# Kernel optimization log

Measured on AMD Instinct MI355X. Metric: run time of the kernel, lower is better.

Reference implementation:

```python
import jax, jax.numpy as jnp
import numpy as np

PROX_THRESH = 50.0
NEG_SLOPE = 0.2  # PyG GATConv default leaky_relu slope


def _layer_norm(x, g, b, eps=1e-5):
    m = x.mean(-1, keepdims=True)
    v = x.var(-1, keepdims=True)
    return (x - m) / jnp.sqrt(v + eps) * g + b


def _forward(ego_agent_past, neighbor_agents_past, node_w, node_b, node_ln_g,
             node_ln_b, ego_w, ego_b, ego_ln_g, ego_ln_b, gat_w, gat_asrc,
             gat_adst, gat_b, proj_w, proj_b):
    B = ego_agent_past.shape[0]
    ego_last = ego_agent_past[:, -1, :5]            # [B,5]
    nbr_last = neighbor_agents_past[:, :, -1, :5]   # [B,Nn,5]
    x = jnp.concatenate([ego_last[:, None], nbr_last], axis=1)  # [B,N,5]
    N = x.shape[1]
    dim = node_w.shape[1]
    heads, C = gat_asrc.shape[1], gat_asrc.shape[2]

    # build_graph: edge (j->i) iff dist(i,j) < 50 and i != j; GATConv then
    # adds self-loops, so the diagonal is always connected.
    pos = x[..., :2]
    d2 = jnp.sum((pos[:, :, None, :] - pos[:, None, :, :]) ** 2, axis=-1)  # [B,N,N]
    eye = jnp.eye(N, dtype=bool)
    adj = ((jnp.sqrt(d2) < PROX_THRESH) & ~eye) | eye   # adj[b,i,j]: msg j -> i

    # node features zero-padded from 5 -> 11 columns (as in forward)
    nf = jnp.pad(x, ((0, 0), (0, 0), (0, 11 - x.shape[-1])))
    h_node = _layer_norm(jax.nn.relu(nf @ node_w + node_b), node_ln_g, node_ln_b)
    h_ego = _layer_norm(jax.nn.relu(nf[..., :7] @ ego_w + ego_b), ego_ln_g, ego_ln_b)
    is_ego = (jnp.arange(N) == 0)  # node 0 of every scene is the ego
    h = jnp.where(is_ego[None, :, None], h_ego, h_node)  # [B,N,dim]

    # GATConv layers (eval mode, dropout inactive), concat=True
    for l in range(gat_w.shape[0]):
        wh = (h @ gat_w[l]).reshape(B, N, heads, C)                    # [B,N,H,C]
        a_s = jnp.einsum('bnhc,hc->bnh', wh, gat_asrc[l])              # source term
        a_d = jnp.einsum('bnhc,hc->bnh', wh, gat_adst[l])              # dest term
        # e[b,i,j,h] for edge j->i
        e = jax.nn.leaky_relu(a_s[:, None, :, :] + a_d[:, :, None, :], NEG_SLOPE)
        e = jnp.where(adj[..., None], e, -1e9)
        alpha = jax.nn.softmax(e, axis=2)                              # over sources j
        out = jnp.einsum('bijh,bjhc->bihc', alpha, wh).reshape(B, N, dim) + gat_b[l]
        h = jax.nn.relu(out)

    h = h @ proj_w + proj_b
    # all agents are valid (randn features have nonzero abs-sum), so no padding
    mask = jnp.zeros((B, N), dtype=bool)
    return h, mask


def setup_inputs() -> dict:
    key = jax.random.key(0)
    ks = jax.random.split(key, 10)
    B, Nn, T = 16, 1023, 20
    dim, heads, L = 256, 4, 2
    C = dim // heads
    f = lambda i, s: jax.random.normal(ks[i], s, dtype=jnp.float32)
    return {
        'ego_agent_past': f(0, (B, T, 7)),
        'neighbor_agents_past': f(1, (B, Nn, T, 11)),
        'node_w': f(2, (11, dim)) * 0.1, 'node_b': jnp.zeros((dim,), jnp.float32),
        'node_ln_g': jnp.ones((dim,), jnp.float32), 'node_ln_b': jnp.zeros((dim,), jnp.float32),
        'ego_w': f(3, (7, dim)) * 0.1, 'ego_b': jnp.zeros((dim,), jnp.float32),
        'ego_ln_g': jnp.ones((dim,), jnp.float32), 'ego_ln_b': jnp.zeros((dim,), jnp.float32),
        'gat_w': f(4, (L, dim, dim)) * 0.1,
        'gat_asrc': f(5, (L, heads, C)) * 0.1,
        'gat_adst': f(6, (L, heads, C)) * 0.1,
        'gat_b': jnp.zeros((L, dim), jnp.float32),
        'proj_w': f(7, (dim, dim)) * 0.1, 'proj_b': jnp.zeros((dim,), jnp.float32),
    }


def reference(ego_agent_past, neighbor_agents_past, node_w, node_b, node_ln_g,
              node_ln_b, ego_w, ego_b, ego_ln_g, ego_ln_b, gat_w, gat_asrc,
              gat_adst, gat_b, proj_w, proj_b):
    return _forward(ego_agent_past, neighbor_agents_past, node_w, node_b,
                    node_ln_g, node_ln_b, ego_w, ego_b, ego_ln_g, ego_ln_b,
                    gat_w, gat_asrc, gat_adst, gat_b, proj_w, proj_b)
```

## Files before the change

### kernel.cpp

```cpp
#include <hip/hip_runtime.h>
#include <cstddef>

typedef _Float16 f16;
typedef _Float16 f16x8 __attribute__((ext_vector_type(8)));
typedef _Float16 f16x4 __attribute__((ext_vector_type(4)));
typedef float f32x4 __attribute__((ext_vector_type(4)));

#define BATCH 16
#define NAGENT 1024
#define NNBR 1023
#define TSTEP 20
#define DIM 256
#define ROWS 16384
#define TH2 2500.0f
#define LOG2E 1.44269504089f

#define O_PX   0
#define O_PY   16384
#define O_H16  32768
#define O_AS   2129920
#define O_AD   2195456
#define O_M    2260992
#define O_US   2261056
#define O_UD   2263104
#define O_WT   2265152
#define O_ADJ  2363456

__global__ __launch_bounds__(256) void node_embed(
    const float* __restrict__ ego, const float* __restrict__ nbr,
    const float* __restrict__ node_w, const float* __restrict__ node_b,
    const float* __restrict__ node_g, const float* __restrict__ node_beta,
    const float* __restrict__ ego_w, const float* __restrict__ ego_b,
    const float* __restrict__ ego_g, const float* __restrict__ ego_beta,
    f16* __restrict__ h16, float* __restrict__ px, float* __restrict__ py) {
    int w = threadIdx.x >> 6, lane = threadIdx.x & 63;
    int row = blockIdx.x * 4 + w;
    int b = row >> 10, n = row & 1023;
    const float* src;
    if (n == 0) src = ego + (size_t)b * TSTEP * 7 + (TSTEP - 1) * 7;
    else        src = nbr + (((size_t)b * NNBR + (n - 1)) * TSTEP + (TSTEP - 1)) * 11;
    const float *W, *bias, *g, *beta;
    if (n == 0) { W = ego_w;  bias = ego_b;  g = ego_g;  beta = ego_beta; }
    else        { W = node_w; bias = node_b; g = node_g; beta = node_beta; }
    float xv[5];
#pragma unroll
    for (int k = 0; k < 5; k++) xv[k] = src[k];
    if (lane == 0) { px[row] = xv[0]; py[row] = xv[1]; }
    int c0 = lane * 4;
    float4 bv = *(const float4*)(bias + c0);
    float acc[4] = {bv.x, bv.y, bv.z, bv.w};
#pragma unroll
    for (int k = 0; k < 5; k++) {
        float4 wv = *(const float4*)(W + (size_t)k * 256 + c0);
        acc[0] = fmaf(xv[k], wv.x, acc[0]);
        acc[1] = fmaf(xv[k], wv.y, acc[1]);
        acc[2] = fmaf(xv[k], wv.z, acc[2]);
        acc[3] = fmaf(xv[k], wv.w, acc[3]);
    }
#pragma unroll
    for (int c = 0; c < 4; c++) acc[c] = fmaxf(acc[c], 0.f);
    float s1 = acc[0] + acc[1] + acc[2] + acc[3];
    float s2 = acc[0]*acc[0] + acc[1]*acc[1] + acc[2]*acc[2] + acc[3]*acc[3];
#pragma unroll
    for (int off = 1; off < 64; off <<= 1) {
        s1 += __shfl_xor(s1, off);
        s2 += __shfl_xor(s2, off);
    }
    float mean = s1 * (1.f / 256.f);
    float var  = s2 * (1.f / 256.f) - mean * mean;
    float rstd = rsqrtf(var + 1e-5f);
    float4 gv = *(const float4*)(g + c0);
    float4 be = *(const float4*)(beta + c0);
    f16x4 o;
    o[0] = (f16)((acc[0] - mean) * rstd * gv.x + be.x);
    o[1] = (f16)((acc[1] - mean) * rstd * gv.y + be.y);
    o[2] = (f16)((acc[2] - mean) * rstd * gv.z + be.z);
    o[3] = (f16)((acc[3] - mean) * rstd * gv.w + be.w);
    *(f16x4*)(h16 + (size_t)row * 256 + c0) = o;
}

__global__ __launch_bounds__(256) void adj_build(const float* __restrict__ px,
                                                 const float* __restrict__ py,
                                                 unsigned char* __restrict__ mask) {
    int blk = blockIdx.x;
    int b = blk >> 6, ic = blk & 63;
    int base = b << 10;
    __shared__ float sx[1024], sy[1024];
    int t = threadIdx.x;
#pragma unroll
    for (int i = 0; i < 4; i++) {
        sx[t + i * 256] = px[base + t + i * 256];
        sy[t + i * 256] = py[base + t + i * 256];
    }
    __syncthreads();
    int i_loc = t >> 4;
    int s = (t >> 3) & 1;
    int q = (t >> 1) & 3;
    int chalf = t & 1;
    int ig = ic * 16 + i_loc;
    float xi = sx[ig], yi = sy[ig];
    unsigned int w0 = 0, w1 = 0;
#pragma unroll
    for (int cc = 0; cc < 8; cc++) {
        int c = chalf * 8 + cc;
        unsigned int byte = 0;
        int j0 = s * 512 + c * 32 + q * 8;
#pragma unroll
        for (int jj = 0; jj < 8; jj++) {
            int j = j0 + jj;
            float dx = sx[j] - xi, dy = sy[j] - yi;
            if ((dx * dx + dy * dy < TH2) || (j == ig)) byte |= 1u << jj;
        }
        if (cc < 4) w0 |= byte << (cc * 8);
        else        w1 |= byte << ((cc - 4) * 8);
    }
    uint2 v; v.x = w0; v.y = w1;
    *(uint2*)(mask + (((size_t)(base + ig)) << 7) + s * 64 + q * 16 + chalf * 8) = v;
}

__global__ __launch_bounds__(256) void prep_weights(
    const float* __restrict__ gat_w, const float* __restrict__ proj_w,
    const float* __restrict__ asrc, const float* __restrict__ adst,
    f16* __restrict__ WT, float* __restrict__ us, float* __restrict__ ud) {
    int bid = blockIdx.x;
    int t = threadIdx.x;
    if (bid < 48) {
        int m = bid >> 4, t4 = bid & 15;
        int ti = (t4 >> 2) * 64;
        int tj = (t4 & 3) * 64;
        const float* W = (m < 2) ? (gat_w + (size_t)m * 65536) : proj_w;
        __shared__ float ls[64][68];
#pragma unroll
        for (int i = 0; i < 4; i++) {
            int idx = t + i * 256;
            int r = idx >> 4, c4 = (idx & 15) * 4;
            float4 v = *(const float4*)(W + (size_t)(ti + r) * 256 + tj + c4);
            ls[r][c4] = v.x; ls[r][c4 + 1] = v.y; ls[r][c4 + 2] = v.z; ls[r][c4 + 3] = v.w;
        }
        __syncthreads();
#pragma unroll
        for (int i = 0; i < 2; i++) {
            int idx = t + i * 256;
            int nr = idx >> 3, kc = (idx & 7) * 8;
            f16x8 v;
#pragma unroll
            for (int j = 0; j < 8; j++) v[j] = (f16)ls[kc + j][nr];
            *(f16x8*)(WT + (size_t)m * 65536 + (size_t)(tj + nr) * 256 + ti + kc) = v;
        }
    } else {
        int blk = bid - 48;
        int l = blk >> 2, h = blk & 3;
        const float* W  = gat_w + (size_t)l * 65536 + t * 256 + h * 64;
        const float* as = asrc + l * 256 + h * 64;
        const float* ad = adst + l * 256 + h * 64;
        float s = 0.f, d = 0.f;
#pragma unroll 8
        for (int c = 0; c < 64; c++) { s = fmaf(W[c], as[c], s); d = fmaf(W[c], ad[c], d); }
        us[blk * 256 + t] = s;
        ud[blk * 256 + t] = d;
    }
}

__global__ __launch_bounds__(256, 4) void gemm_f16(
    const f16* __restrict__ A, const f16* __restrict__ BT,
    f16* __restrict__ whT, float* __restrict__ outF, const float* __restrict__ bias,
    const float* __restrict__ us, const float* __restrict__ ud,
    float* __restrict__ a_sT, float* __restrict__ a_dT) {
    __shared__ f16 sA[32 * 264];
    __shared__ float sU[8 * 256];
    int t = threadIdx.x;
    int m0 = blockIdx.x * 32;
    {
        int r = t >> 3, u0 = (t & 7) * 4;
        const f16* gp = A + (size_t)(m0 + r) * 256 + u0 * 8;
        f16* lp = sA + r * 264 + u0 * 8;
#pragma unroll
        for (int u = 0; u < 4; u++)
            *(f16x8*)(lp + u * 8) = *(const f16x8*)(gp + u * 8);
    }
    if (us) {
#pragma unroll
        for (int i = 0; i < 4; i++) sU[t + i * 256] = us[t + i * 256];
#pragma unroll
        for (int i = 0; i < 4; i++) sU[1024 + t + i * 256] = ud[t + i * 256];
    }
    __syncthreads();
    int w = t >> 6, lane = t & 63, il = lane & 15, q = lane >> 4;
    int n0 = w * 64;
    f32x4 acc[2][4];
#pragma unroll
    for (int mt = 0; mt < 2; mt++)
#pragma unroll
        for (int nt = 0; nt < 4; nt++) acc[mt][nt] = (f32x4){0.f, 0.f, 0.f, 0.f};
    const f16* Bp  = BT + (size_t)(n0 + il) * 256 + q * 8;
    const f16* Ap0 = sA + il * 264 + q * 8;
#pragma unroll 2
    for (int ks = 0; ks < 256; ks += 32) {
        f16x8 a0 = *(const f16x8*)(Ap0 + ks);
        f16x8 a1 = *(const f16x8*)(Ap0 + 16 * 264 + ks);
        f16x8 b0 = *(const f16x8*)(Bp + ks);
        f16x8 b1 = *(const f16x8*)(Bp + 16 * 256 + ks);
        f16x8 b2 = *(const f16x8*)(Bp + 32 * 256 + ks);
        f16x8 b3 = *(const f16x8*)(Bp + 48 * 256 + ks);
        acc[0][0] = __builtin_amdgcn_mfma_f32_16x16x32_f16(a0, b0, acc[0][0], 0, 0, 0);
        acc[0][1] = __builtin_amdgcn_mfma_f32_16x16x32_f16(a0, b1, acc[0][1], 0, 0, 0);
        acc[0][2] = __builtin_amdgcn_mfma_f32_16x16x32_f16(a0, b2, acc[0][2], 0, 0, 0);
        acc[0][3] = __builtin_amdgcn_mfma_f32_16x16x32_f16(a0, b3, acc[0][3], 0, 0, 0);
        acc[1][0] = __builtin_amdgcn_mfma_f32_16x16x32_f16(a1, b0, acc[1][0], 0, 0, 0);
        acc[1][1] = __builtin_amdgcn_mfma_f32_16x16x32_f16(a1, b1, acc[1][1], 0, 0, 0);
        acc[1][2] = __builtin_amdgcn_mfma_f32_16x16x32_f16(a1, b2, acc[1][2], 0, 0, 0);
        acc[1][3] = __builtin_amdgcn_mfma_f32_16x16x32_f16(a1, b3, acc[1][3], 0, 0, 0);
    }
    if (whT) {
#pragma unroll
        for (int mt = 0; mt < 2; mt++)
#pragma unroll
            for (int nt = 0; nt < 4; nt++) {
                f16x4 v;
#pragma unroll
                for (int reg = 0; reg < 4; reg++) v[reg] = (f16)acc[mt][nt][reg];
                *(f16x4*)(whT + (size_t)(n0 + nt * 16 + il) * ROWS + m0 + mt * 16 + q * 4) = v;
            }
    } else {
#pragma unroll
        for (int nt = 0; nt < 4; nt++) {
            float bv = bias[n0 + nt * 16 + il];
#pragma unroll
            for (int mt = 0; mt < 2; mt++)
#pragma unroll
                for (int reg = 0; reg < 4; reg++)
                    outF[(size_t)(m0 + mt * 16 + q * 4 + reg) * 256 + n0 + nt * 16 + il] =
                        acc[mt][nt][reg] + bv;
        }
    }
    if (us) {
        int r2 = t >> 3, sub = t & 7;
        int hh = sub & 3, isD = sub >> 2;
        const float* uv = sU + isD * 1024 + hh * 256;
        const f16* ar = sA + r2 * 264;
        float d0 = 0.f;
#pragma unroll 4
        for (int kk = 0; kk < 32; kk++) {
            f16x8 av = *(const f16x8*)(ar + kk * 8);
            float4 u0 = *(const float4*)(uv + kk * 8);
            float4 u1 = *(const float4*)(uv + kk * 8 + 4);
            d0 += (float)av[0] * u0.x + (float)av[1] * u0.y +
                  (float)av[2] * u0.z + (float)av[3] * u0.w +
                  (float)av[4] * u1.x + (float)av[5] * u1.y +
                  (float)av[6] * u1.z + (float)av[7] * u1.w;
        }
        float* dst = isD ? a_dT : a_sT;
        dst[(size_t)hh * ROWS + m0 + r2] = d0;
    }
}

__global__ __launch_bounds__(256) void reduce_max(const float* __restrict__ a_sT,
                                                  float* __restrict__ M) {
    int blk = blockIdx.x;
    int b = blk >> 2, h = blk & 3;
    const float* p = a_sT + (size_t)h * ROWS + b * NAGENT;
    int t = threadIdx.x;
    float m = fmaxf(fmaxf(p[t], p[t + 256]), fmaxf(p[t + 512], p[t + 768]));
#pragma unroll
    for (int off = 32; off > 0; off >>= 1) m = fmaxf(m, __shfl_down(m, off));
    __shared__ float red[4];
    if ((t & 63) == 0) red[t >> 6] = m;
    __syncthreads();
    if (t == 0) M[blk] = fmaxf(fmaxf(red[0], red[1]), fmaxf(red[2], red[3]));
}

__global__ __launch_bounds__(512, 4) void gat_attn(
    const f16* __restrict__ whT, const float* __restrict__ a_sT,
    const float* __restrict__ a_dT, const unsigned char* __restrict__ mask,
    const float* __restrict__ M, const float* __restrict__ gat_b,
    f16* __restrict__ h16out) {
    __shared__ f32x4 comb[4][64][10];
    int t = threadIdx.x;
    int w = t >> 6, lane = t & 63;
    int h = w & 3, s = w >> 2;
    int blk = blockIdx.x;
    int b = blk >> 5;
    int i0 = (blk & 31) << 5;
    int base = b << 10;
    int il = lane & 15, q = lane >> 4;
    int ig0 = i0 + il, ig1 = i0 + 16 + il;

    float Mh = M[b * 4 + h];
    float adv0 = a_dT[(size_t)h * ROWS + base + ig0];
    float adv1 = a_dT[(size_t)h * ROWS + base + ig1];
    float mz0 = Mh + adv0, mz1 = Mh + adv1;
    float mi0 = fmaxf(mz0, 0.2f * mz0), mi1 = fmaxf(mz1, 0.2f * mz1);
    float nm0 = -mi0 * LOG2E, nm1 = -mi1 * LOG2E;

    uint4 mq0 = *(const uint4*)(mask + (((size_t)(base + ig0)) << 7) + s * 64 + q * 16);
    uint4 mq1 = *(const uint4*)(mask + (((size_t)(base + ig1)) << 7) + s * 64 + q * 16);
    unsigned int mw0[4] = {mq0.x, mq0.y, mq0.z, mq0.w};
    unsigned int mw1[4] = {mq1.x, mq1.y, mq1.z, mq1.w};

    f32x4 acc[2][5];
#pragma unroll
    for (int mt = 0; mt < 2; mt++)
#pragma unroll
        for (int nt = 0; nt < 5; nt++) acc[mt][nt] = (f32x4){0.f, 0.f, 0.f, 0.f};
    f16x8 ones;
#pragma unroll
    for (int j = 0; j < 8; j++) ones[j] = (f16)1.f;

    int jbase = base + (s << 9);
    const f16*   wp  = whT + (size_t)(h * 64 + il) * ROWS + jbase + q * 8;
    const float* asp = a_sT + (size_t)h * ROWS + jbase + q * 8;

    for (int c = 0; c < 16; ++c) {
        int j0 = c * 32;
        f16x8 b0 = *(const f16x8*)(wp + j0);
        f16x8 b1 = *(const f16x8*)(wp + (size_t)16 * ROWS + j0);
        f16x8 b2 = *(const f16x8*)(wp + (size_t)32 * ROWS + j0);
        f16x8 b3 = *(const f16x8*)(wp + (size_t)48 * ROWS + j0);
        float4 as0 = *(const float4*)(asp + j0);
        float4 as1 = *(const float4*)(asp + j0 + 4);
        unsigned int mb0 = (mw0[c >> 2] >> ((c & 3) * 8)) & 255u;
        unsigned int mb1 = (mw1[c >> 2] >> ((c & 3) * 8)) & 255u;
        float asv[8] = {as0.x, as0.y, as0.z, as0.w, as1.x, as1.y, as1.z, as1.w};
        f16x8 afr0, afr1;
#pragma unroll
        for (int jj = 0; jj < 8; ++jj) {
            float z = asv[jj];
            float z0 = z + adv0, z1 = z + adv1;
            float sc0 = fmaxf(z0, 0.2f * z0), sc1 = fmaxf(z1, 0.2f * z1);
            float e0 = exp2f(fmaf(sc0, LOG2E, nm0));
            float e1 = exp2f(fmaf(sc1, LOG2E, nm1));
            afr0[jj] = (f16)(((mb0 >> jj) & 1u) ? e0 : 0.f);
            afr1[jj] = (f16)(((mb1 >> jj) & 1u) ? e1 : 0.f);
        }
        acc[0][0] = __builtin_amdgcn_mfma_f32_16x16x32_f16(afr0, b0, acc[0][0], 0, 0, 0);
        acc[1][0] = __builtin_amdgcn_mfma_f32_16x16x32_f16(afr1, b0, acc[1][0], 0, 0, 0);
        acc[0][1] = __builtin_amdgcn_mfma_f32_16x16x32_f16(afr0, b1, acc[0][1], 0, 0, 0);
        acc[1][1] = __builtin_amdgcn_mfma_f32_16x16x32_f16(afr1, b1, acc[1][1], 0, 0, 0);
        acc[0][2] = __builtin_amdgcn_mfma_f32_16x16x32_f16(afr0, b2, acc[0][2], 0, 0, 0);
        acc[1][2] = __builtin_amdgcn_mfma_f32_16x16x32_f16(afr1, b2, acc[1][2], 0, 0, 0);
        acc[0][3] = __builtin_amdgcn_mfma_f32_16x16x32_f16(afr0, b3, acc[0][3], 0, 0, 0);
        acc[1][3] = __builtin_amdgcn_mfma_f32_16x16x32_f16(afr1, b3, acc[1][3], 0, 0, 0);
        acc[0][4] = __builtin_amdgcn_mfma_f32_16x16x32_f16(afr0, ones, acc[0][4], 0, 0, 0);
        acc[1][4] = __builtin_amdgcn_mfma_f32_16x16x32_f16(afr1, ones, acc[1][4], 0, 0, 0);
    }
    if (s == 1) {
#pragma unroll
        for (int mt = 0; mt < 2; mt++)
#pragma unroll
            for (int nt = 0; nt < 5; nt++) comb[h][lane][mt * 5 + nt] = acc[mt][nt];
    }
    __syncthreads();
    if (s == 0) {
#pragma unroll
        for (int mt = 0; mt < 2; mt++)
#pragma unroll
            for (int nt = 0; nt < 5; nt++) acc[mt][nt] += comb[h][lane][mt * 5 + nt];
        float b0v = gat_b[h * 64 + il];
        float b1v = gat_b[h * 64 + 16 + il];
        float b2v = gat_b[h * 64 + 32 + il];
        float b3v = gat_b[h * 64 + 48 + il];
#pragma unroll
        for (int mt = 0; mt < 2; mt++) {
#pragma unroll
            for (int reg = 0; reg < 4; ++reg) {
                float inv = 1.f / acc[mt][4][reg];
                size_t ro = (size_t)(base + i0 + mt * 16 + q * 4 + reg) * DIM + h * 64 + il;
                h16out[ro +  0] = (f16)fmaxf(fmaf(acc[mt][0][reg], inv, b0v), 0.f);
                h16out[ro + 16] = (f16)fmaxf(fmaf(acc[mt][1][reg], inv, b1v), 0.f);
                h16out[ro + 32] = (f16)fmaxf(fmaf(acc[mt][2][reg], inv, b2v), 0.f);
                h16out[ro + 48] = (f16)fmaxf(fmaf(acc[mt][3][reg], inv, b3v), 0.f);
            }
        }
    }
}

__global__ void zero_mask(float* __restrict__ p) {
    p[blockIdx.x * 256 + threadIdx.x] = 0.f;
}

extern "C" void kernel_launch(void* const* d_in, const int* in_sizes, int n_in,
                              void* d_out, int out_size, void* d_ws, size_t ws_size,
                              hipStream_t stream) {
    const float* ego       = (const float*)d_in[0];
    const float* nbr       = (const float*)d_in[1];
    const float* node_w    = (const float*)d_in[2];
    const float* node_b    = (const float*)d_in[3];
    const float* node_g    = (const float*)d_in[4];
    const float* node_beta = (const float*)d_in[5];
    const float* ego_w     = (const float*)d_in[6];
    const float* ego_b     = (const float*)d_in[7];
    const float* ego_g     = (const float*)d_in[8];
    const float* ego_beta  = (const float*)d_in[9];
    const float* gat_w     = (const float*)d_in[10];
    const float* gat_asrc  = (const float*)d_in[11];
    const float* gat_adst  = (const float*)d_in[12];
    const float* gat_bias  = (const float*)d_in[13];
    const float* proj_w    = (const float*)d_in[14];
    const float* proj_b    = (const float*)d_in[15];

    float* out = (float*)d_out;
    float* ws  = (float*)d_ws;
    float* px   = ws + O_PX;
    float* py   = ws + O_PY;
    f16*   h16  = (f16*)(ws + O_H16);
    float* asT  = ws + O_AS;
    float* adT  = ws + O_AD;
    float* Mmax = ws + O_M;
    float* us   = ws + O_US;
    float* ud   = ws + O_UD;
    f16*   WT   = (f16*)(ws + O_WT);
    unsigned char* adj = (unsigned char*)(ws + O_ADJ);
    f16*   whT  = (f16*)d_out;

    node_embed<<<4096, 256, 0, stream>>>(ego, nbr, node_w, node_b, node_g, node_beta,
                                         ego_w, ego_b, ego_g, ego_beta, h16, px, py);
    adj_build<<<1024, 256, 0, stream>>>(px, py, adj);
    prep_weights<<<56, 256, 0, stream>>>(gat_w, proj_w, gat_asrc, gat_adst, WT, us, ud);
    for (int l = 0; l < 2; l++) {
        gemm_f16<<<512, 256, 0, stream>>>(h16, WT + (size_t)l * 65536, whT, nullptr, nullptr,
                                          us + l * 1024, ud + l * 1024, asT, adT);
        reduce_max<<<64, 256, 0, stream>>>(asT, Mmax);
        gat_attn<<<512, 512, 0, stream>>>(whT, asT, adT, adj, Mmax,
                                          gat_bias + l * 256, h16);
    }
    gemm_f16<<<512, 256, 0, stream>>>(h16, WT + (size_t)2 * 65536, nullptr, out, proj_b,
                                      nullptr, nullptr, nullptr, nullptr);
    zero_mask<<<64, 256, 0, stream>>>(out + (size_t)ROWS * DIM);
}
```

Before: 252.4 us.

## Halve GEMM row tile, pack exp conversions, transpose attention combine buffer

The GEMM now gives each block 16 rows instead of 32 and launches 1024 blocks, which adds parallelism across CUs but loads each B tile twice as often. The attention softmax weights are converted in pairs with packed round-toward-zero f16 conversion instead of per-element casts. The shared combine buffer is transposed so that lanes access consecutive addresses, avoiding LDS bank conflicts. The rtz rounding slightly changes the numerics.

```diff
diff --git a/kernel.cpp b/kernel.cpp
--- a/kernel.cpp
+++ b/kernel.cpp
@@ -4,6 +4,7 @@
 typedef _Float16 f16;
 typedef _Float16 f16x8 __attribute__((ext_vector_type(8)));
 typedef _Float16 f16x4 __attribute__((ext_vector_type(4)));
+typedef __fp16 fp16x2 __attribute__((ext_vector_type(2)));
 typedef float f32x4 __attribute__((ext_vector_type(4)));
 
 #define BATCH 16
@@ -166,17 +167,16 @@
     f16* __restrict__ whT, float* __restrict__ outF, const float* __restrict__ bias,
     const float* __restrict__ us, const float* __restrict__ ud,
     float* __restrict__ a_sT, float* __restrict__ a_dT) {
-    __shared__ f16 sA[32 * 264];
+    __shared__ f16 sA[16 * 264];
     __shared__ float sU[8 * 256];
     int t = threadIdx.x;
-    int m0 = blockIdx.x * 32;
+    int m0 = blockIdx.x * 16;
     {
-        int r = t >> 3, u0 = (t & 7) * 4;
-        const f16* gp = A + (size_t)(m0 + r) * 256 + u0 * 8;
-        f16* lp = sA + r * 264 + u0 * 8;
-#pragma unroll
-        for (int u = 0; u < 4; u++)
-            *(f16x8*)(lp + u * 8) = *(const f16x8*)(gp + u * 8);
+        int r = t >> 4, u0 = (t & 15) * 16;
+        const f16* gp = A + (size_t)(m0 + r) * 256 + u0;
+        f16* lp = sA + r * 264 + u0;
+        *(f16x8*)lp = *(const f16x8*)gp;
+        *(f16x8*)(lp + 8) = *(const f16x8*)(gp + 8);
     }
     if (us) {
 #pragma unroll
@@ -187,70 +187,61 @@
     __syncthreads();
     int w = t >> 6, lane = t & 63, il = lane & 15, q = lane >> 4;
     int n0 = w * 64;
-    f32x4 acc[2][4];
-#pragma unroll
-    for (int mt = 0; mt < 2; mt++)
-#pragma unroll
-        for (int nt = 0; nt < 4; nt++) acc[mt][nt] = (f32x4){0.f, 0.f, 0.f, 0.f};
+    f32x4 acc[4];
+#pragma unroll
+    for (int nt = 0; nt < 4; nt++) acc[nt] = (f32x4){0.f, 0.f, 0.f, 0.f};
     const f16* Bp  = BT + (size_t)(n0 + il) * 256 + q * 8;
     const f16* Ap0 = sA + il * 264 + q * 8;
 #pragma unroll 2
     for (int ks = 0; ks < 256; ks += 32) {
         f16x8 a0 = *(const f16x8*)(Ap0 + ks);
-        f16x8 a1 = *(const f16x8*)(Ap0 + 16 * 264 + ks);
         f16x8 b0 = *(const f16x8*)(Bp + ks);
         f16x8 b1 = *(const f16x8*)(Bp + 16 * 256 + ks);
         f16x8 b2 = *(const f16x8*)(Bp + 32 * 256 + ks);
         f16x8 b3 = *(const f16x8*)(Bp + 48 * 256 + ks);
-        acc[0][0] = __builtin_amdgcn_mfma_f32_16x16x32_f16(a0, b0, acc[0][0], 0, 0, 0);
-        acc[0][1] = __builtin_amdgcn_mfma_f32_16x16x32_f16(a0, b1, acc[0][1], 0, 0, 0);
-        acc[0][2] = __builtin_amdgcn_mfma_f32_16x16x32_f16(a0, b2, acc[0][2], 0, 0, 0);
-        acc[0][3] = __builtin_amdgcn_mfma_f32_16x16x32_f16(a0, b3, acc[0][3], 0, 0, 0);
-        acc[1][0] = __builtin_amdgcn_mfma_f32_16x16x32_f16(a1, b0, acc[1][0], 0, 0, 0);
-        acc[1][1] = __builtin_amdgcn_mfma_f32_16x16x32_f16(a1, b1, acc[1][1], 0, 0, 0);
-        acc[1][2] = __builtin_amdgcn_mfma_f32_16x16x32_f16(a1, b2, acc[1][2], 0, 0, 0);
-        acc[1][3] = __builtin_amdgcn_mfma_f32_16x16x32_f16(a1, b3, acc[1][3], 0, 0, 0);
+        acc[0] = __builtin_amdgcn_mfma_f32_16x16x32_f16(a0, b0, acc[0], 0, 0, 0);
+        acc[1] = __builtin_amdgcn_mfma_f32_16x16x32_f16(a0, b1, acc[1], 0, 0, 0);
+        acc[2] = __builtin_amdgcn_mfma_f32_16x16x32_f16(a0, b2, acc[2], 0, 0, 0);
+        acc[3] = __builtin_amdgcn_mfma_f32_16x16x32_f16(a0, b3, acc[3], 0, 0, 0);
     }
     if (whT) {
 #pragma unroll
-        for (int mt = 0; mt < 2; mt++)
-#pragma unroll
-            for (int nt = 0; nt < 4; nt++) {
-                f16x4 v;
-#pragma unroll
-                for (int reg = 0; reg < 4; reg++) v[reg] = (f16)acc[mt][nt][reg];
-                *(f16x4*)(whT + (size_t)(n0 + nt * 16 + il) * ROWS + m0 + mt * 16 + q * 4) = v;
-            }
+        for (int nt = 0; nt < 4; nt++) {
+            f16x4 v;
+#pragma unroll
+            for (int reg = 0; reg < 4; reg++) v[reg] = (f16)acc[nt][reg];
+            *(f16x4*)(whT + (size_t)(n0 + nt * 16 + il) * ROWS + m0 + q * 4) = v;
+        }
     } else {
 #pragma unroll
         for (int nt = 0; nt < 4; nt++) {
             float bv = bias[n0 + nt * 16 + il];
 #pragma unroll
-            for (int mt = 0; mt < 2; mt++)
-#pragma unroll
-                for (int reg = 0; reg < 4; reg++)
-                    outF[(size_t)(m0 + mt * 16 + q * 4 + reg) * 256 + n0 + nt * 16 + il] =
-                        acc[mt][nt][reg] + bv;
+            for (int reg = 0; reg < 4; reg++)
+                outF[(size_t)(m0 + q * 4 + reg) * 256 + n0 + nt * 16 + il] =
+                    acc[nt][reg] + bv;
         }
     }
     if (us) {
-        int r2 = t >> 3, sub = t & 7;
-        int hh = sub & 3, isD = sub >> 2;
-        const float* uv = sU + isD * 1024 + hh * 256;
-        const f16* ar = sA + r2 * 264;
-        float d0 = 0.f;
+        int r2 = t >> 4, sub = t & 15;
+        if (sub < 8) {
+            int hh = sub & 3, isD = sub >> 2;
+            const float* uv = sU + isD * 1024 + hh * 256;
+            const f16* ar = sA + r2 * 264;
+            float d0 = 0.f;
 #pragma unroll 4
-        for (int kk = 0; kk < 32; kk++) {
-            f16x8 av = *(const f16x8*)(ar + kk * 8);
-            float4 u0 = *(const float4*)(uv + kk * 8);
-            float4 u1 = *(const float4*)(uv + kk * 8 + 4);
-            d0 += (float)av[0] * u0.x + (float)av[1] * u0.y +
-                  (float)av[2] * u0.z + (float)av[3] * u0.w +
-                  (float)av[4] * u1.x + (float)av[5] * u1.y +
-                  (float)av[6] * u1.z + (float)av[7] * u1.w;
-        }
-        float* dst = isD ? a_dT : a_sT;
-        dst[(size_t)hh * ROWS + m0 + r2] = d0;
+            for (int kk = 0; kk < 32; kk++) {
+                f16x8 av = *(const f16x8*)(ar + kk * 8);
+                float4 u0 = *(const float4*)(uv + kk * 8);
+                float4 u1 = *(const float4*)(uv + kk * 8 + 4);
+                d0 += (float)av[0] * u0.x + (float)av[1] * u0.y +
+                      (float)av[2] * u0.z + (float)av[3] * u0.w +
+                      (float)av[4] * u1.x + (float)av[5] * u1.y +
+                      (float)av[6] * u1.z + (float)av[7] * u1.w;
+            }
+            float* dst = isD ? a_dT : a_sT;
+            dst[(size_t)hh * ROWS + m0 + r2] = d0;
+        }
     }
 }
 
@@ -274,7 +265,7 @@
     const float* __restrict__ a_dT, const unsigned char* __restrict__ mask,
     const float* __restrict__ M, const float* __restrict__ gat_b,
     f16* __restrict__ h16out) {
-    __shared__ f32x4 comb[4][64][10];
+    __shared__ f32x4 comb[10][4][64];
     int t = threadIdx.x;
     int w = t >> 6, lane = t & 63;
     int h = w & 3, s = w >> 2;
@@ -321,17 +312,26 @@
         unsigned int mb0 = (mw0[c >> 2] >> ((c & 3) * 8)) & 255u;
         unsigned int mb1 = (mw1[c >> 2] >> ((c & 3) * 8)) & 255u;
         float asv[8] = {as0.x, as0.y, as0.z, as0.w, as1.x, as1.y, as1.z, as1.w};
-        f16x8 afr0, afr1;
-#pragma unroll
-        for (int jj = 0; jj < 8; ++jj) {
-            float z = asv[jj];
-            float z0 = z + adv0, z1 = z + adv1;
-            float sc0 = fmaxf(z0, 0.2f * z0), sc1 = fmaxf(z1, 0.2f * z1);
-            float e0 = exp2f(fmaf(sc0, LOG2E, nm0));
-            float e1 = exp2f(fmaf(sc1, LOG2E, nm1));
-            afr0[jj] = (f16)(((mb0 >> jj) & 1u) ? e0 : 0.f);
-            afr1[jj] = (f16)(((mb1 >> jj) & 1u) ? e1 : 0.f);
-        }
+        union { f16x8 v; fp16x2 hp[4]; } u0, u1;
+#pragma unroll
+        for (int jp = 0; jp < 4; ++jp) {
+            float va = asv[2 * jp], vb = asv[2 * jp + 1];
+            float za = va + adv0, zb = vb + adv0;
+            float zc = va + adv1, zd = vb + adv1;
+            float sa = fmaxf(za, 0.2f * za), sb = fmaxf(zb, 0.2f * zb);
+            float sc_ = fmaxf(zc, 0.2f * zc), sd = fmaxf(zd, 0.2f * zd);
+            float ea = exp2f(fmaf(sa, LOG2E, nm0));
+            float eb = exp2f(fmaf(sb, LOG2E, nm0));
+            float ec = exp2f(fmaf(sc_, LOG2E, nm1));
+            float ed = exp2f(fmaf(sd, LOG2E, nm1));
+            ea = ((mb0 >> (2 * jp)) & 1u) ? ea : 0.f;
+            eb = ((mb0 >> (2 * jp + 1)) & 1u) ? eb : 0.f;
+            ec = ((mb1 >> (2 * jp)) & 1u) ? ec : 0.f;
+            ed = ((mb1 >> (2 * jp + 1)) & 1u) ? ed : 0.f;
+            u0.hp[jp] = __builtin_amdgcn_cvt_pkrtz(ea, eb);
+            u1.hp[jp] = __builtin_amdgcn_cvt_pkrtz(ec, ed);
+        }
+        f16x8 afr0 = u0.v, afr1 = u1.v;
         acc[0][0] = __builtin_amdgcn_mfma_f32_16x16x32_f16(afr0, b0, acc[0][0], 0, 0, 0);
         acc[1][0] = __builtin_amdgcn_mfma_f32_16x16x32_f16(afr1, b0, acc[1][0], 0, 0, 0);
         acc[0][1] = __builtin_amdgcn_mfma_f32_16x16x32_f16(afr0, b1, acc[0][1], 0, 0, 0);
@@ -347,14 +347,14 @@
 #pragma unroll
         for (int mt = 0; mt < 2; mt++)
 #pragma unroll
-            for (int nt = 0; nt < 5; nt++) comb[h][lane][mt * 5 + nt] = acc[mt][nt];
+            for (int nt = 0; nt < 5; nt++) comb[mt * 5 + nt][h][lane] = acc[mt][nt];
     }
     __syncthreads();
     if (s == 0) {
 #pragma unroll
         for (int mt = 0; mt < 2; mt++)
 #pragma unroll
-            for (int nt = 0; nt < 5; nt++) acc[mt][nt] += comb[h][lane][mt * 5 + nt];
+            for (int nt = 0; nt < 5; nt++) acc[mt][nt] += comb[mt * 5 + nt][h][lane];
         float b0v = gat_b[h * 64 + il];
         float b1v = gat_b[h * 64 + 16 + il];
         float b2v = gat_b[h * 64 + 32 + il];
@@ -417,13 +417,13 @@
     adj_build<<<1024, 256, 0, stream>>>(px, py, adj);
     prep_weights<<<56, 256, 0, stream>>>(gat_w, proj_w, gat_asrc, gat_adst, WT, us, ud);
     for (int l = 0; l < 2; l++) {
-        gemm_f16<<<512, 256, 0, stream>>>(h16, WT + (size_t)l * 65536, whT, nullptr, nullptr,
-                                          us + l * 1024, ud + l * 1024, asT, adT);
+        gemm_f16<<<1024, 256, 0, stream>>>(h16, WT + (size_t)l * 65536, whT, nullptr, nullptr,
+                                           us + l * 1024, ud + l * 1024, asT, adT);
         reduce_max<<<64, 256, 0, stream>>>(asT, Mmax);
         gat_attn<<<512, 512, 0, stream>>>(whT, asT, adT, adj, Mmax,
                                           gat_bias + l * 256, h16);
     }
-    gemm_f16<<<512, 256, 0, stream>>>(h16, WT + (size_t)2 * 65536, nullptr, out, proj_b,
-                                      nullptr, nullptr, nullptr, nullptr);
+    gemm_f16<<<1024, 256, 0, stream>>>(h16, WT + (size_t)2 * 65536, nullptr, out, proj_b,
+                                       nullptr, nullptr, nullptr, nullptr);
     zero_mask<<<64, 256, 0, stream>>>(out + (size_t)ROWS * DIM);
 }
```

New measurement: 275.6 us. 9.2% more time.
